# Kernel optimization log

Hardware: AMD Instinct MI355X
Metric: run time of the kernel (lower is better)

## Reference

```python
import jax, jax.numpy as jnp
import numpy as np

INF = 1e10
D_KEY = 64

def setup_inputs() -> dict:
    key = jax.random.key(0)
    k1, k2, k3 = jax.random.split(key, 3)
    B, S, D = 4, 4096, D_KEY
    return {
        "query": jax.random.normal(k1, (B, S, D), dtype=jnp.float32),
        "key": jax.random.normal(k2, (B, S, D), dtype=jnp.float32),
        "value": jax.random.normal(k3, (B, S, D), dtype=jnp.float32),
        "mask": jnp.ones((B, S), dtype=jnp.float32),
    }

def reference(query, key, value, mask):
    # dot_products: [B, Sq, Sk]
    dot = jnp.einsum('bqd,bkd->bqk', query, key)
    S = key.shape[1]
    # causal: subtract INF on strict upper triangle (triu(1))
    tri = jnp.triu(jnp.ones((S, S), dtype=dot.dtype), 1) * INF
    dot = dot - tri[None, :, :]
    # additive padding mask: subtract (1-mask)*INF broadcast over query dim
    dot = dot - (1.0 - mask)[:, None, :] * INF
    scale = jnp.sqrt(jnp.float32(D_KEY))
    probs = jax.nn.softmax(dot / scale, axis=-1)  # [B, Sq, Sk]
    # dropout ratio = 0.0 -> identity
    return jnp.einsum('bqk,bkd->bqd', probs, value)
```

## Files before the change

### kernel.cpp

```cpp
#include <hip/hip_runtime.h>
#include <hip/hip_bf16.h>


#define S_LEN  4096
#define N_B    4
#define NT64   64
#define BIGF   1.803368e9f
#define QSCALE (0.125f * 1.44269504089f)
#define FIXMAX 11.0f
#define BIGNEG 1.25e9f
#define MADD_PAD 4224

typedef __attribute__((ext_vector_type(8))) short short8;
typedef __attribute__((ext_vector_type(4))) float f32x4;
typedef __attribute__((ext_vector_type(2))) unsigned int uint2v;
typedef unsigned short ushort_t;

#define KT2_OFF   0
#define KT2_BYTES (N_B * NT64 * 4096 * 2)
#define VT2_OFF   (KT2_OFF + KT2_BYTES)
#define VT2_BYTES (N_B * NT64 * 4096 * 2)
#define NSLOT     (N_B * 368 * 4)
#define OP_OFF    (VT2_OFF + VT2_BYTES)
#define OP_BYTES  (NSLOT * 512 * 4)
#define PLS_OFF   (OP_OFF + OP_BYTES)
#define PLS_BYTES (NSLOT * 16 * 4)
#define MADD_OFF  (PLS_OFF + PLS_BYTES)
#define MADD_BYTES (N_B * MADD_PAD * 4)
#define FLAG_OFF  (MADD_OFF + MADD_BYTES)
#define WS5_NEEDED (FLAG_OFF + 64)

__device__ __forceinline__ unsigned short f2bf(float f) {
    union { float f; unsigned u; } v; v.f = f;
    unsigned r = v.u + 0x7FFF + ((v.u >> 16) & 1);
    return (unsigned short)(r >> 16);
}
__device__ __forceinline__ float bflo(unsigned u) {
    union { unsigned u; float f; } v; v.u = u << 16; return v.f;
}
__device__ __forceinline__ float bfhi(unsigned u) {
    union { unsigned u; float f; } v; v.u = u & 0xffff0000u; return v.f;
}
__device__ __forceinline__ void ld_lds16(const void* g, void* l) {
    __builtin_amdgcn_global_load_lds((const __attribute__((address_space(1))) void*)g,
                                     (__attribute__((address_space(3))) void*)l, 16, 0, 0);
}


__global__ __launch_bounds__(256)
void prep5(const float* __restrict__ K, const float* __restrict__ V,
           const float* __restrict__ M,
           ushort_t* __restrict__ Kt, ushort_t* __restrict__ Vt,
           float* __restrict__ Madd, unsigned* __restrict__ Flag)
{
    const int t = blockIdx.x, b = blockIdx.y, tid = threadIdx.x;
    ushort_t* ko = Kt + ((size_t)(b * NT64 + t)) * 4096;
    ushort_t* vo = Vt + ((size_t)(b * NT64 + t)) * 4096;
    #pragma unroll
    for (int i = 0; i < 2; ++i) {
        const int idx = tid + 256 * i;
        const int row = idx >> 3, cc = idx & 7;
        const float* src = K + ((size_t)(b * S_LEN + t * 64 + row)) * 64 + cc * 8;
        const f32x4 a = *(const f32x4*)src;
        const f32x4 d4 = *(const f32x4*)(src + 4);
        short8 w;
        w[0]=(short)f2bf(a[0]); w[1]=(short)f2bf(a[1]); w[2]=(short)f2bf(a[2]); w[3]=(short)f2bf(a[3]);
        w[4]=(short)f2bf(d4[0]); w[5]=(short)f2bf(d4[1]); w[6]=(short)f2bf(d4[2]); w[7]=(short)f2bf(d4[3]);
        *(short8*)(ko + row * 64 + ((cc ^ (row & 7)) << 3)) = w;
    }
    #pragma unroll
    for (int i = 0; i < 2; ++i) {
        const int idx = tid + 256 * i;
        const int cc = idx >> 6, d = idx & 63;
        short8 w;
        #pragma unroll
        for (int j = 0; j < 8; ++j)
            w[j] = (short)f2bf(V[((size_t)(b * S_LEN + t * 64 + cc * 8 + j)) * 64 + d]);
        *(short8*)(vo + d * 64 + ((cc ^ (d & 7)) << 3)) = w;
    }
    if (tid < 64) {
        const int k = t * 64 + tid;
        const float mv = M[b * S_LEN + k];
        Madd[b * MADD_PAD + k] = (1.0f - mv) * BIGF;
        const unsigned long long nz = __ballot(mv != 1.0f);
        if (tid == 0 && nz) atomicOr(Flag, 1u);
    }
}

#define PTRANS(PA, PB, PF) do {                                                     \
    unsigned c00_, c01_, c10_, c11_;                                                \
    __asm__("v_cvt_pk_bf16_f32 %0, %1, %2" : "=v"(c00_) : "v"(PA[0]), "v"(PA[1])); \
    __asm__("v_cvt_pk_bf16_f32 %0, %1, %2" : "=v"(c01_) : "v"(PA[2]), "v"(PA[3])); \
    __asm__("v_cvt_pk_bf16_f32 %0, %1, %2" : "=v"(c10_) : "v"(PB[0]), "v"(PB[1])); \
    __asm__("v_cvt_pk_bf16_f32 %0, %1, %2" : "=v"(c11_) : "v"(PB[2]), "v"(PB[3])); \
    uint2v s0_ = __builtin_amdgcn_permlane32_swap(c00_, c10_, false, false);        \
    uint2v s1_ = __builtin_amdgcn_permlane32_swap(c01_, c11_, false, false);        \
    const unsigned T0_ = (unsigned)__builtin_amdgcn_ds_swizzle((int)s0_.x, 0x401F); \
    const unsigned T1_ = (unsigned)__builtin_amdgcn_ds_swizzle((int)s1_.x, 0x401F); \
    const unsigned U0_ = (unsigned)__builtin_amdgcn_ds_swizzle((int)s0_.y, 0x401F); \
    const unsigned U1_ = (unsigned)__builtin_amdgcn_ds_swizzle((int)s1_.y, 0x401F); \
    union { unsigned u[4]; short8 s; } pw_;                                         \
    pw_.u[0] = evn ? s0_.x : U0_;                                                   \
    pw_.u[1] = evn ? s1_.x : U1_;                                                   \
    pw_.u[2] = evn ? T0_ : s0_.y;                                                   \
    pw_.u[3] = evn ? T1_ : s1_.y;                                                   \
    PF = pw_.s;                                                                     \
} while (0)

__global__ __launch_bounds__(256)
void attn_fa8(const float* __restrict__ Q, const ushort_t* __restrict__ Kt,
              const ushort_t* __restrict__ Vt, const float* __restrict__ Madd,
              const unsigned* __restrict__ Flag,
              unsigned* __restrict__ Opu, float* __restrict__ Pll,
              float* __restrict__ O)
{
    const int x = 373 - blockIdx.x;
    const int b = blockIdx.y;
    int v = 1;
    #pragma unroll
    for (int vv = 2; vv <= 11; ++vv) v += (x >= 3 * vv * (vv - 1)) ? 1 : 0;
    const int y  = x - 3 * v * (v - 1);
    const int T  = 6 * (v - 1) + y / v;
    const int c  = y - (y / v) * v;
    const int t0 = 6 * c;
    const int tmax = T + 1;
    const int t1 = (t0 + 6 < tmax) ? t0 + 6 : tmax;

    const unsigned anymask = *Flag;

    const int wid  = threadIdx.x >> 6;
    const int lane = threadIdx.x & 63, l15 = lane & 15, g = lane >> 4;
    const bool evn = ((lane & 16) == 0);
    const int qbase = T * 64 + wid * 16;

    __shared__ __attribute__((aligned(16))) ushort_t Kb[2][4096];
    __shared__ __attribute__((aligned(16))) ushort_t Vb[2][4096];

    const float* Qrow = Q + ((size_t)(b * S_LEN + qbase + l15)) * 64 + g * 8;
    const f32x4 qa = *(const f32x4*)(Qrow);
    const f32x4 qb_ = *(const f32x4*)(Qrow + 4);
    const f32x4 qc = *(const f32x4*)(Qrow + 32);
    const f32x4 qd = *(const f32x4*)(Qrow + 36);
    short8 qf0, qf1;
    #pragma unroll
    for (int j = 0; j < 4; ++j) {
        qf0[j]     = (short)f2bf(qa[j]  * QSCALE);
        qf0[4 + j] = (short)f2bf(qb_[j] * QSCALE);
        qf1[j]     = (short)f2bf(qc[j]  * QSCALE);
        qf1[4 + j] = (short)f2bf(qd[j]  * QSCALE);
    }
    short8 ones8;
    #pragma unroll
    for (int j = 0; j < 8; ++j) ones8[j] = (short)0x3F80;

    const char*  KtB = (const char*)Kt + (size_t)b * (NT64 * 8192);
    const char*  VtB = (const char*)Vt + (size_t)b * (NT64 * 8192);
    const float* MaB = Madd + (size_t)b * MADD_PAD + 4 * g;

    f32x4 acc[5];
    #pragma unroll
    for (int dt = 0; dt < 5; ++dt) acc[dt] = (f32x4){0.f, 0.f, 0.f, 0.f};

    auto stage = [&](int bf, int t_) {
        const char* kg = KtB + (size_t)t_ * 8192 + wid * 2048 + lane * 16;
        char* kl = (char*)&Kb[bf][0] + wid * 2048;
        ld_lds16(kg,        kl);
        ld_lds16(kg + 1024, kl + 1024);
        const char* vg = VtB + (size_t)t_ * 8192 + wid * 2048 + lane * 16;
        char* vl = (char*)&Vb[bf][0] + wid * 2048;
        ld_lds16(vg,        vl);
        ld_lds16(vg + 1024, vl + 1024);
    };

    stage(0, t0);
    int buf = 0;
    const int ch0 = ((g ^ (l15 & 7)) << 3);
    const int ch1 = (((4 | g) ^ (l15 & 7)) << 3);

    for (int t = t0; t < t1; ++t) {
        f32x4 mm0, mm1, mm2, mm3;
        if (anymask) {
            const float* mp = MaB + t * 64;
            mm0 = *(const f32x4*)(mp);
            mm1 = *(const f32x4*)(mp + 16);
            mm2 = *(const f32x4*)(mp + 32);
            mm3 = *(const f32x4*)(mp + 48);
        }
        if (t + 1 < t1) {
            stage(buf ^ 1, t + 1);
            __asm__ volatile("s_waitcnt vmcnt(4)" ::: "memory");
        } else {
            __asm__ volatile("s_waitcnt vmcnt(0)" ::: "memory");
        }
        __builtin_amdgcn_s_barrier();
        __builtin_amdgcn_sched_barrier(0);

        const ushort_t* kb = &Kb[buf][0];
        const f32x4 z_ = (f32x4){0.f, 0.f, 0.f, 0.f};
        short8 k00 = *(const short8*)(kb + ((0  + l15) << 6) + ch0);
        short8 k01 = *(const short8*)(kb + ((0  + l15) << 6) + ch1);
        short8 k10 = *(const short8*)(kb + ((16 + l15) << 6) + ch0);
        short8 k11 = *(const short8*)(kb + ((16 + l15) << 6) + ch1);
        short8 k20 = *(const short8*)(kb + ((32 + l15) << 6) + ch0);
        short8 k21 = *(const short8*)(kb + ((32 + l15) << 6) + ch1);
        short8 k30 = *(const short8*)(kb + ((48 + l15) << 6) + ch0);
        short8 k31 = *(const short8*)(kb + ((48 + l15) << 6) + ch1);
        f32x4 st0 = __builtin_amdgcn_mfma_f32_16x16x32_bf16(k00, qf0, z_, 0, 0, 0);
        f32x4 st1 = __builtin_amdgcn_mfma_f32_16x16x32_bf16(k10, qf0, z_, 0, 0, 0);
        f32x4 st2 = __builtin_amdgcn_mfma_f32_16x16x32_bf16(k20, qf0, z_, 0, 0, 0);
        f32x4 st3 = __builtin_amdgcn_mfma_f32_16x16x32_bf16(k30, qf0, z_, 0, 0, 0);
        st0 = __builtin_amdgcn_mfma_f32_16x16x32_bf16(k01, qf1, st0, 0, 0, 0);
        st1 = __builtin_amdgcn_mfma_f32_16x16x32_bf16(k11, qf1, st1, 0, 0, 0);
        st2 = __builtin_amdgcn_mfma_f32_16x16x32_bf16(k21, qf1, st2, 0, 0, 0);
        st3 = __builtin_amdgcn_mfma_f32_16x16x32_bf16(k31, qf1, st3, 0, 0, 0);

        if (anymask) {
            st0 -= mm0; st1 -= mm1; st2 -= mm2; st3 -= mm3;
        }
        if (t == T) {
            const int qg = 16 * wid + l15 - 4 * g;
            #pragma unroll
            for (int r = 0; r < 4; ++r) {
                if (r > qg)      st0[r] -= BIGF;
                if (16 + r > qg) st1[r] -= BIGF;
                if (32 + r > qg) st2[r] -= BIGF;
                if (48 + r > qg) st3[r] -= BIGF;
            }
        }

        float p0[4], p1[4], p2[4], p3[4];
        #pragma unroll
        for (int r = 0; r < 4; ++r) {
            p0[r] = exp2f(st0[r] - FIXMAX);
            p1[r] = exp2f(st1[r] - FIXMAX);
            p2[r] = exp2f(st2[r] - FIXMAX);
            p3[r] = exp2f(st3[r] - FIXMAX);
        }

        short8 pfA, pfB;
        PTRANS(p0, p1, pfA);
        PTRANS(p2, p3, pfB);

        const ushort_t* vb = &Vb[buf][0];
        short8 vA0 = *(const short8*)(vb + ((0  + l15) << 6) + ch0);
        short8 vB0 = *(const short8*)(vb + ((0  + l15) << 6) + ch1);
        short8 vA1 = *(const short8*)(vb + ((16 + l15) << 6) + ch0);
        short8 vB1 = *(const short8*)(vb + ((16 + l15) << 6) + ch1);
        short8 vA2 = *(const short8*)(vb + ((32 + l15) << 6) + ch0);
        short8 vB2 = *(const short8*)(vb + ((32 + l15) << 6) + ch1);
        short8 vA3 = *(const short8*)(vb + ((48 + l15) << 6) + ch0);
        short8 vB3 = *(const short8*)(vb + ((48 + l15) << 6) + ch1);
        __builtin_amdgcn_s_setprio(1);
        acc[0] = __builtin_amdgcn_mfma_f32_16x16x32_bf16(pfA, vA0, acc[0], 0, 0, 0);
        acc[1] = __builtin_amdgcn_mfma_f32_16x16x32_bf16(pfA, vA1, acc[1], 0, 0, 0);
        acc[2] = __builtin_amdgcn_mfma_f32_16x16x32_bf16(pfA, vA2, acc[2], 0, 0, 0);
        acc[3] = __builtin_amdgcn_mfma_f32_16x16x32_bf16(pfA, vA3, acc[3], 0, 0, 0);
        acc[4] = __builtin_amdgcn_mfma_f32_16x16x32_bf16(pfA, ones8, acc[4], 0, 0, 0);
        acc[0] = __builtin_amdgcn_mfma_f32_16x16x32_bf16(pfB, vB0, acc[0], 0, 0, 0);
        acc[1] = __builtin_amdgcn_mfma_f32_16x16x32_bf16(pfB, vB1, acc[1], 0, 0, 0);
        acc[2] = __builtin_amdgcn_mfma_f32_16x16x32_bf16(pfB, vB2, acc[2], 0, 0, 0);
        acc[3] = __builtin_amdgcn_mfma_f32_16x16x32_bf16(pfB, vB3, acc[3], 0, 0, 0);
        acc[4] = __builtin_amdgcn_mfma_f32_16x16x32_bf16(pfB, ones8, acc[4], 0, 0, 0);
        __builtin_amdgcn_s_setprio(0);

        __builtin_amdgcn_sched_barrier(0);
        __builtin_amdgcn_s_barrier();
        buf ^= 1;
    }

    if (v == 1) {
        float* Ob = O + ((size_t)(b * S_LEN + qbase)) * 64;
        #pragma unroll
        for (int r = 0; r < 4; ++r) {
            const float il = 1.0f / acc[4][r];
            #pragma unroll
            for (int dt = 0; dt < 4; ++dt)
                Ob[(4 * g + r) * 64 + 16 * dt + l15] = acc[dt][r] * il;
        }
    } else {
        const int slot = (b * 368 + (x - 6)) * 4 + wid;
        unsigned* Os = Opu + (size_t)slot * 512;
        #pragma unroll
        for (int dt = 0; dt < 4; ++dt) {
            unsigned plo, phi;
            __asm__("v_cvt_pk_bf16_f32 %0, %1, %2" : "=v"(plo) : "v"(acc[dt][0]), "v"(acc[dt][1]));
            __asm__("v_cvt_pk_bf16_f32 %0, %1, %2" : "=v"(phi) : "v"(acc[dt][2]), "v"(acc[dt][3]));
            *(uint2v*)&Os[(16 * dt + l15) * 8 + g * 2] = (uint2v){plo, phi};
        }
        if (l15 == 0) {
            #pragma unroll
            for (int r = 0; r < 4; ++r)
                Pll[slot * 16 + 4 * g + r] = acc[4][r];
        }
    }
}

__global__ __launch_bounds__(256)
void combine5(const unsigned* __restrict__ Opu, const float* __restrict__ Pll,
              float* __restrict__ O)
{
    const int bx = blockIdx.x, b = blockIdx.y;
    const int T = 6 + (bx >> 2), w = bx & 3;
    const int v = (T + 6) / 6;
    const int x0 = 3 * v * (v - 1) + (T - 6 * (v - 1)) * v;
    const int sb = (b * 368 + (x0 - 6)) * 4 + w;
    const int tid = threadIdx.x, rg = tid >> 6, d = tid & 63;

    float l[4] = {0.f, 0.f, 0.f, 0.f};
    float a[4] = {0.f, 0.f, 0.f, 0.f};
    for (int cc = 0; cc < v; ++cc) {
        const int sl = sb + 4 * cc;
        #pragma unroll
        for (int j = 0; j < 4; ++j)
            l[j] += Pll[sl * 16 + 4 * rg + j];
        const uint2v pu = *(const uint2v*)&Opu[(size_t)sl * 512 + d * 8 + rg * 2];
        a[0] += bflo(pu[0]);
        a[1] += bfhi(pu[0]);
        a[2] += bflo(pu[1]);
        a[3] += bfhi(pu[1]);
    }
    float* Ob = O + ((size_t)(b * S_LEN + T * 64 + w * 16 + 4 * rg)) * 64 + d;
    #pragma unroll
    for (int j = 0; j < 4; ++j)
        Ob[(size_t)j * 64] = a[j] / l[j];
}


__global__ __launch_bounds__(256)
void attn_fwd_fb(const float* __restrict__ Q, const float* __restrict__ K,
                 const float* __restrict__ V, const float* __restrict__ M,
                 float* __restrict__ O)
{
    const int tile  = blockIdx.x;
    const int b     = blockIdx.y;
    const int qbase = tile * 64;
    const int tid   = threadIdx.x;
    const int wave  = tid >> 6;
    const int lane  = tid & 63;
    const int l15   = lane & 15;
    const int g     = lane >> 4;

    __shared__ __attribute__((aligned(16))) unsigned short Klds[32 * 64];
    __shared__ __attribute__((aligned(16))) unsigned short Vtlds[64 * 40];
    __shared__ __attribute__((aligned(16))) unsigned short Plds[4][16 * 40];

    const float* Qb = Q + ((size_t)b * S_LEN + qbase) * 64;
    const float* Kb = K + (size_t)b * S_LEN * 64;
    const float* Vb = V + (size_t)b * S_LEN * 64;
    const float* Mb = M + (size_t)b * S_LEN;

    const int qrow = 16 * wave + l15;
    short8 qf[2];
    #pragma unroll
    for (int dc = 0; dc < 2; ++dc) {
        const float* src = Qb + (size_t)qrow * 64 + dc * 32 + g * 8;
        #pragma unroll
        for (int j = 0; j < 8; ++j) qf[dc][j] = (short)f2bf(src[j] * 0.125f);
    }

    f32x4 acc[4];
    #pragma unroll
    for (int dt = 0; dt < 4; ++dt) acc[dt] = (f32x4){0.f, 0.f, 0.f, 0.f};
    float mrow[4], lrow[4];
    #pragma unroll
    for (int r = 0; r < 4; ++r) { mrow[r] = -1e30f; lrow[r] = 0.f; }

    const int q_max_wave = qbase + 16 * wave + 15;
    const int nkv = (qbase + 64) / 32;

    for (int it = 0; it < nkv; ++it) {
        const int kv = it * 32;
        __syncthreads();
        {
            const int k = tid >> 3, c = tid & 7;
            const float* src = Kb + (size_t)(kv + k) * 64 + c * 8;
            short8 t8;
            #pragma unroll
            for (int j = 0; j < 8; ++j) t8[j] = (short)f2bf(src[j]);
            const int byte = k * 128 + ((c * 16) ^ ((k & 7) << 4));
            *(short8*)((char*)Klds + byte) = t8;
        }
        {
            const int k = tid & 31, dch = tid >> 5;
            const float* src = Vb + (size_t)(kv + k) * 64 + dch * 8;
            #pragma unroll
            for (int j = 0; j < 8; ++j)
                Vtlds[(dch * 8 + j) * 40 + k] = f2bf(src[j]);
        }
        __syncthreads();

        if (kv > q_max_wave) continue;

        f32x4 s[2];
        s[0] = (f32x4){0.f,0.f,0.f,0.f};
        s[1] = (f32x4){0.f,0.f,0.f,0.f};
        #pragma unroll
        for (int kt = 0; kt < 2; ++kt) {
            const int krow = 16 * kt + l15;
            #pragma unroll
            for (int dc = 0; dc < 2; ++dc) {
                const int byte = krow * 128 + ((dc * 64 + g * 16) ^ ((krow & 7) << 4));
                short8 kf = *(const short8*)((const char*)Klds + byte);
                s[kt] = __builtin_amdgcn_mfma_f32_16x16x32_bf16(qf[dc], kf, s[kt], 0, 0, 0);
            }
        }

        float mk0 = Mb[kv + l15];
        float mk1 = Mb[kv + 16 + l15];
        #pragma unroll
        for (int kt = 0; kt < 2; ++kt) {
            const int gk = kv + 16 * kt + l15;
            const float madd = (1.0f - (kt ? mk1 : mk0)) * BIGNEG;
            #pragma unroll
            for (int r = 0; r < 4; ++r) {
                const int gq = qbase + 16 * wave + 4 * g + r;
                float vv = s[kt][r] - madd;
                if (gk > gq) vv -= BIGNEG;
                s[kt][r] = vv;
            }
        }

        float pexp[2][4], alpha[4];
        #pragma unroll
        for (int r = 0; r < 4; ++r) {
            float tm = fmaxf(s[0][r], s[1][r]);
            #pragma unroll
            for (int off = 8; off >= 1; off >>= 1)
                tm = fmaxf(tm, __shfl_xor(tm, off, 64));
            const float mnew = fmaxf(mrow[r], tm);
            const float a  = __expf(mrow[r] - mnew);
            const float p0 = __expf(s[0][r] - mnew);
            const float p1 = __expf(s[1][r] - mnew);
            float rs = p0 + p1;
            #pragma unroll
            for (int off = 8; off >= 1; off >>= 1)
                rs += __shfl_xor(rs, off, 64);
            lrow[r] = lrow[r] * a + rs;
            mrow[r] = mnew;
            alpha[r] = a;
            pexp[0][r] = p0; pexp[1][r] = p1;
        }

        #pragma unroll
        for (int dt = 0; dt < 4; ++dt)
            #pragma unroll
            for (int r = 0; r < 4; ++r)
                acc[dt][r] *= alpha[r];

        unsigned short* P = Plds[wave];
        #pragma unroll
        for (int kt = 0; kt < 2; ++kt)
            #pragma unroll
            for (int r = 0; r < 4; ++r)
                P[(4 * g + r) * 40 + 16 * kt + l15] = f2bf(pexp[kt][r]);

        __asm__ volatile("s_waitcnt lgkmcnt(0)" ::: "memory");

        short8 pf = *(const short8*)((const char*)P + (l15 * 40 + g * 8) * 2);
        #pragma unroll
        for (int dt = 0; dt < 4; ++dt) {
            short8 vf = *(const short8*)((const char*)Vtlds + ((dt * 16 + l15) * 40 + g * 8) * 2);
            acc[dt] = __builtin_amdgcn_mfma_f32_16x16x32_bf16(pf, vf, acc[dt], 0, 0, 0);
        }
    }

    float* Ob = O + ((size_t)b * S_LEN + qbase) * 64;
    #pragma unroll
    for (int r = 0; r < 4; ++r) {
        const float inv = 1.0f / lrow[r];
        const int row = 16 * wave + 4 * g + r;
        #pragma unroll
        for (int dt = 0; dt < 4; ++dt)
            Ob[(size_t)row * 64 + dt * 16 + l15] = acc[dt][r] * inv;
    }
}

extern "C" void kernel_launch(void* const* d_in, const int* in_sizes, int n_in,
                              void* d_out, int out_size, void* d_ws, size_t ws_size,
                              hipStream_t stream) {
    const float* Q = (const float*)d_in[0];
    const float* K = (const float*)d_in[1];
    const float* V = (const float*)d_in[2];
    const float* M = (const float*)d_in[3];
    float* O = (float*)d_out;

    if (ws_size >= (size_t)WS5_NEEDED) {
        ushort_t* Kt = (ushort_t*)((char*)d_ws + KT2_OFF);
        ushort_t* Vt = (ushort_t*)((char*)d_ws + VT2_OFF);
        unsigned* Op = (unsigned*)((char*)d_ws + OP_OFF);
        float*    Pll= (float*)((char*)d_ws + PLS_OFF);
        float*    Ma = (float*)((char*)d_ws + MADD_OFF);
        unsigned* Fl = (unsigned*)((char*)d_ws + FLAG_OFF);
        hipMemsetAsync(Fl, 0, 4, stream);
        prep5<<<dim3(NT64, N_B), 256, 0, stream>>>(K, V, M, Kt, Vt, Ma, Fl);
        attn_fa8<<<dim3(374, N_B), 256, 0, stream>>>(Q, Kt, Vt, Ma, Fl, Op, Pll, O);
        combine5<<<dim3(232, N_B), 256, 0, stream>>>(Op, Pll, O);
    } else {
        dim3 grid(S_LEN / 64, N_B);
        attn_fwd_fb<<<grid, 256, 0, stream>>>(Q, K, V, M, O);
    }
}
```

Baseline: 45.59 us.

## Double query tile per block to 128 rows, halving grid and split slots

Each block now covers 128 query rows, with each wave holding two 16-row query fragments, so every K/V tile loaded into LDS serves twice as many queries. The grid and split-K schedule are rebuilt for 128-row tiles (187 blocks per batch, 184 partial slots). Waves whose diagonal tile has already been passed skip their compute through a liveness flag. The combine kernel is rewritten for the new partial layout. Register pressure rises with twice the accumulators, launch bounds now ask for 3 blocks per unit, and the grid has fewer blocks to spread across CUs.

```diff
diff --git a/kernel.cpp b/kernel.cpp
--- a/kernel.cpp
+++ b/kernel.cpp
@@ -14,21 +14,22 @@
 typedef __attribute__((ext_vector_type(8))) short short8;
 typedef __attribute__((ext_vector_type(4))) float f32x4;
 typedef __attribute__((ext_vector_type(2))) unsigned int uint2v;
+typedef __attribute__((ext_vector_type(4))) unsigned int uint4v;
 typedef unsigned short ushort_t;
 
 #define KT2_OFF   0
 #define KT2_BYTES (N_B * NT64 * 4096 * 2)
 #define VT2_OFF   (KT2_OFF + KT2_BYTES)
 #define VT2_BYTES (N_B * NT64 * 4096 * 2)
-#define NSLOT     (N_B * 368 * 4)
+#define NSLOT     (N_B * 184 * 4)
 #define OP_OFF    (VT2_OFF + VT2_BYTES)
-#define OP_BYTES  (NSLOT * 512 * 4)
+#define OP_BYTES  (NSLOT * 1024 * 4)
 #define PLS_OFF   (OP_OFF + OP_BYTES)
-#define PLS_BYTES (NSLOT * 16 * 4)
+#define PLS_BYTES (NSLOT * 32 * 4)
 #define MADD_OFF  (PLS_OFF + PLS_BYTES)
 #define MADD_BYTES (N_B * MADD_PAD * 4)
 #define FLAG_OFF  (MADD_OFF + MADD_BYTES)
-#define WS5_NEEDED (FLAG_OFF + 64)
+#define WS6_NEEDED (FLAG_OFF + 64)
 
 __device__ __forceinline__ unsigned short f2bf(float f) {
     union { float f; unsigned u; } v; v.f = f;
@@ -107,47 +108,67 @@
     PF = pw_.s;                                                                     \
 } while (0)
 
-__global__ __launch_bounds__(256)
-void attn_fa8(const float* __restrict__ Q, const ushort_t* __restrict__ Kt,
+#define CMASK(SV, BB, QG) do {                     \
+    _Pragma("unroll")                              \
+    for (int r_ = 0; r_ < 4; ++r_)                 \
+        if ((BB) + r_ > (QG)) SV[r_] -= BIGF;      \
+} while (0)
+
+__global__ __launch_bounds__(256, 3)
+void attn_fa9(const float* __restrict__ Q, const ushort_t* __restrict__ Kt,
               const ushort_t* __restrict__ Vt, const float* __restrict__ Madd,
               const unsigned* __restrict__ Flag,
               unsigned* __restrict__ Opu, float* __restrict__ Pll,
               float* __restrict__ O)
 {
-    const int x = 373 - blockIdx.x;
+    const int x = 186 - blockIdx.x;
     const int b = blockIdx.y;
     int v = 1;
     #pragma unroll
-    for (int vv = 2; vv <= 11; ++vv) v += (x >= 3 * vv * (vv - 1)) ? 1 : 0;
-    const int y  = x - 3 * v * (v - 1);
-    const int T  = 6 * (v - 1) + y / v;
+    for (int vv = 2; vv <= 11; ++vv) v += (x >= (3 * vv * (vv - 1)) / 2) ? 1 : 0;
+    const int y  = x - (3 * v * (v - 1)) / 2;
+    const int T  = 3 * (v - 1) + y / v;
     const int c  = y - (y / v) * v;
+    const int nt = 2 * T + 2;
     const int t0 = 6 * c;
-    const int tmax = T + 1;
-    const int t1 = (t0 + 6 < tmax) ? t0 + 6 : tmax;
+    const int t1 = (t0 + 6 < nt) ? t0 + 6 : nt;
 
     const unsigned anymask = *Flag;
 
     const int wid  = threadIdx.x >> 6;
     const int lane = threadIdx.x & 63, l15 = lane & 15, g = lane >> 4;
     const bool evn = ((lane & 16) == 0);
-    const int qbase = T * 64 + wid * 16;
+    const int qbase = T * 128 + wid * 32;
+    const int dtile = 2 * T + (wid >> 1);
+    const int qg0 = 32 * (wid & 1) + l15 - 4 * g;
+    const int qg1 = qg0 + 16;
 
     __shared__ __attribute__((aligned(16))) ushort_t Kb[2][4096];
     __shared__ __attribute__((aligned(16))) ushort_t Vb[2][4096];
 
-    const float* Qrow = Q + ((size_t)(b * S_LEN + qbase + l15)) * 64 + g * 8;
-    const f32x4 qa = *(const f32x4*)(Qrow);
-    const f32x4 qb_ = *(const f32x4*)(Qrow + 4);
-    const f32x4 qc = *(const f32x4*)(Qrow + 32);
-    const f32x4 qd = *(const f32x4*)(Qrow + 36);
-    short8 qf0, qf1;
-    #pragma unroll
-    for (int j = 0; j < 4; ++j) {
-        qf0[j]     = (short)f2bf(qa[j]  * QSCALE);
-        qf0[4 + j] = (short)f2bf(qb_[j] * QSCALE);
-        qf1[j]     = (short)f2bf(qc[j]  * QSCALE);
-        qf1[4 + j] = (short)f2bf(qd[j]  * QSCALE);
+    const float* Q0 = Q + ((size_t)(b * S_LEN + qbase + l15)) * 64 + g * 8;
+    short8 qA0, qA1, qB0, qB1;
+    {
+        const f32x4 a0 = *(const f32x4*)(Q0);
+        const f32x4 a1 = *(const f32x4*)(Q0 + 4);
+        const f32x4 a2 = *(const f32x4*)(Q0 + 32);
+        const f32x4 a3 = *(const f32x4*)(Q0 + 36);
+        const float* Q1 = Q0 + 16 * 64;
+        const f32x4 b0 = *(const f32x4*)(Q1);
+        const f32x4 b1 = *(const f32x4*)(Q1 + 4);
+        const f32x4 b2 = *(const f32x4*)(Q1 + 32);
+        const f32x4 b3 = *(const f32x4*)(Q1 + 36);
+        #pragma unroll
+        for (int j = 0; j < 4; ++j) {
+            qA0[j]     = (short)f2bf(a0[j] * QSCALE);
+            qA0[4 + j] = (short)f2bf(a1[j] * QSCALE);
+            qA1[j]     = (short)f2bf(a2[j] * QSCALE);
+            qA1[4 + j] = (short)f2bf(a3[j] * QSCALE);
+            qB0[j]     = (short)f2bf(b0[j] * QSCALE);
+            qB0[4 + j] = (short)f2bf(b1[j] * QSCALE);
+            qB1[j]     = (short)f2bf(b2[j] * QSCALE);
+            qB1[4 + j] = (short)f2bf(b3[j] * QSCALE);
+        }
     }
     short8 ones8;
     #pragma unroll
@@ -157,9 +178,12 @@
     const char*  VtB = (const char*)Vt + (size_t)b * (NT64 * 8192);
     const float* MaB = Madd + (size_t)b * MADD_PAD + 4 * g;
 
-    f32x4 acc[5];
-    #pragma unroll
-    for (int dt = 0; dt < 5; ++dt) acc[dt] = (f32x4){0.f, 0.f, 0.f, 0.f};
+    f32x4 accA[5], accB[5];
+    #pragma unroll
+    for (int dt = 0; dt < 5; ++dt) {
+        accA[dt] = (f32x4){0.f, 0.f, 0.f, 0.f};
+        accB[dt] = (f32x4){0.f, 0.f, 0.f, 0.f};
+    }
 
     auto stage = [&](int bf, int t_) {
         const char* kg = KtB + (size_t)t_ * 8192 + wid * 2048 + lane * 16;
@@ -178,8 +202,9 @@
     const int ch1 = (((4 | g) ^ (l15 & 7)) << 3);
 
     for (int t = t0; t < t1; ++t) {
+        const bool live = (t <= dtile);
         f32x4 mm0, mm1, mm2, mm3;
-        if (anymask) {
+        if (anymask && live) {
             const float* mp = MaB + t * 64;
             mm0 = *(const f32x4*)(mp);
             mm1 = *(const f32x4*)(mp + 16);
@@ -195,73 +220,98 @@
         __builtin_amdgcn_s_barrier();
         __builtin_amdgcn_sched_barrier(0);
 
-        const ushort_t* kb = &Kb[buf][0];
-        const f32x4 z_ = (f32x4){0.f, 0.f, 0.f, 0.f};
-        short8 k00 = *(const short8*)(kb + ((0  + l15) << 6) + ch0);
-        short8 k01 = *(const short8*)(kb + ((0  + l15) << 6) + ch1);
-        short8 k10 = *(const short8*)(kb + ((16 + l15) << 6) + ch0);
-        short8 k11 = *(const short8*)(kb + ((16 + l15) << 6) + ch1);
-        short8 k20 = *(const short8*)(kb + ((32 + l15) << 6) + ch0);
-        short8 k21 = *(const short8*)(kb + ((32 + l15) << 6) + ch1);
-        short8 k30 = *(const short8*)(kb + ((48 + l15) << 6) + ch0);
-        short8 k31 = *(const short8*)(kb + ((48 + l15) << 6) + ch1);
-        f32x4 st0 = __builtin_amdgcn_mfma_f32_16x16x32_bf16(k00, qf0, z_, 0, 0, 0);
-        f32x4 st1 = __builtin_amdgcn_mfma_f32_16x16x32_bf16(k10, qf0, z_, 0, 0, 0);
-        f32x4 st2 = __builtin_amdgcn_mfma_f32_16x16x32_bf16(k20, qf0, z_, 0, 0, 0);
-        f32x4 st3 = __builtin_amdgcn_mfma_f32_16x16x32_bf16(k30, qf0, z_, 0, 0, 0);
-        st0 = __builtin_amdgcn_mfma_f32_16x16x32_bf16(k01, qf1, st0, 0, 0, 0);
-        st1 = __builtin_amdgcn_mfma_f32_16x16x32_bf16(k11, qf1, st1, 0, 0, 0);
-        st2 = __builtin_amdgcn_mfma_f32_16x16x32_bf16(k21, qf1, st2, 0, 0, 0);
-        st3 = __builtin_amdgcn_mfma_f32_16x16x32_bf16(k31, qf1, st3, 0, 0, 0);
-
-        if (anymask) {
-            st0 -= mm0; st1 -= mm1; st2 -= mm2; st3 -= mm3;
-        }
-        if (t == T) {
-            const int qg = 16 * wid + l15 - 4 * g;
+        if (live) {
+            const ushort_t* kb = &Kb[buf][0];
+            const f32x4 z_ = (f32x4){0.f, 0.f, 0.f, 0.f};
+            short8 k00 = *(const short8*)(kb + ((0  + l15) << 6) + ch0);
+            short8 k01 = *(const short8*)(kb + ((0  + l15) << 6) + ch1);
+            short8 k10 = *(const short8*)(kb + ((16 + l15) << 6) + ch0);
+            short8 k11 = *(const short8*)(kb + ((16 + l15) << 6) + ch1);
+            short8 k20 = *(const short8*)(kb + ((32 + l15) << 6) + ch0);
+            short8 k21 = *(const short8*)(kb + ((32 + l15) << 6) + ch1);
+            short8 k30 = *(const short8*)(kb + ((48 + l15) << 6) + ch0);
+            short8 k31 = *(const short8*)(kb + ((48 + l15) << 6) + ch1);
+
+            f32x4 sA0 = __builtin_amdgcn_mfma_f32_16x16x32_bf16(k00, qA0, z_, 0, 0, 0);
+            f32x4 sA1 = __builtin_amdgcn_mfma_f32_16x16x32_bf16(k10, qA0, z_, 0, 0, 0);
+            f32x4 sA2 = __builtin_amdgcn_mfma_f32_16x16x32_bf16(k20, qA0, z_, 0, 0, 0);
+            f32x4 sA3 = __builtin_amdgcn_mfma_f32_16x16x32_bf16(k30, qA0, z_, 0, 0, 0);
+            f32x4 sB0 = __builtin_amdgcn_mfma_f32_16x16x32_bf16(k00, qB0, z_, 0, 0, 0);
+            f32x4 sB1 = __builtin_amdgcn_mfma_f32_16x16x32_bf16(k10, qB0, z_, 0, 0, 0);
+            f32x4 sB2 = __builtin_amdgcn_mfma_f32_16x16x32_bf16(k20, qB0, z_, 0, 0, 0);
+            f32x4 sB3 = __builtin_amdgcn_mfma_f32_16x16x32_bf16(k30, qB0, z_, 0, 0, 0);
+            sA0 = __builtin_amdgcn_mfma_f32_16x16x32_bf16(k01, qA1, sA0, 0, 0, 0);
+            sA1 = __builtin_amdgcn_mfma_f32_16x16x32_bf16(k11, qA1, sA1, 0, 0, 0);
+            sA2 = __builtin_amdgcn_mfma_f32_16x16x32_bf16(k21, qA1, sA2, 0, 0, 0);
+            sA3 = __builtin_amdgcn_mfma_f32_16x16x32_bf16(k31, qA1, sA3, 0, 0, 0);
+            sB0 = __builtin_amdgcn_mfma_f32_16x16x32_bf16(k01, qB1, sB0, 0, 0, 0);
+            sB1 = __builtin_amdgcn_mfma_f32_16x16x32_bf16(k11, qB1, sB1, 0, 0, 0);
+            sB2 = __builtin_amdgcn_mfma_f32_16x16x32_bf16(k21, qB1, sB2, 0, 0, 0);
+            sB3 = __builtin_amdgcn_mfma_f32_16x16x32_bf16(k31, qB1, sB3, 0, 0, 0);
+
+            if (anymask) {
+                sA0 -= mm0; sA1 -= mm1; sA2 -= mm2; sA3 -= mm3;
+                sB0 -= mm0; sB1 -= mm1; sB2 -= mm2; sB3 -= mm3;
+            }
+            if (t == dtile) {
+                CMASK(sA0, 0, qg0); CMASK(sA1, 16, qg0);
+                CMASK(sA2, 32, qg0); CMASK(sA3, 48, qg0);
+                CMASK(sB0, 0, qg1); CMASK(sB1, 16, qg1);
+                CMASK(sB2, 32, qg1); CMASK(sB3, 48, qg1);
+            }
+
+            float pa0[4], pa1[4], pa2[4], pa3[4];
+            float pb0[4], pb1[4], pb2[4], pb3[4];
             #pragma unroll
             for (int r = 0; r < 4; ++r) {
-                if (r > qg)      st0[r] -= BIGF;
-                if (16 + r > qg) st1[r] -= BIGF;
-                if (32 + r > qg) st2[r] -= BIGF;
-                if (48 + r > qg) st3[r] -= BIGF;
-            }
-        }
-
-        float p0[4], p1[4], p2[4], p3[4];
-        #pragma unroll
-        for (int r = 0; r < 4; ++r) {
-            p0[r] = exp2f(st0[r] - FIXMAX);
-            p1[r] = exp2f(st1[r] - FIXMAX);
-            p2[r] = exp2f(st2[r] - FIXMAX);
-            p3[r] = exp2f(st3[r] - FIXMAX);
-        }
-
-        short8 pfA, pfB;
-        PTRANS(p0, p1, pfA);
-        PTRANS(p2, p3, pfB);
-
-        const ushort_t* vb = &Vb[buf][0];
-        short8 vA0 = *(const short8*)(vb + ((0  + l15) << 6) + ch0);
-        short8 vB0 = *(const short8*)(vb + ((0  + l15) << 6) + ch1);
-        short8 vA1 = *(const short8*)(vb + ((16 + l15) << 6) + ch0);
-        short8 vB1 = *(const short8*)(vb + ((16 + l15) << 6) + ch1);
-        short8 vA2 = *(const short8*)(vb + ((32 + l15) << 6) + ch0);
-        short8 vB2 = *(const short8*)(vb + ((32 + l15) << 6) + ch1);
-        short8 vA3 = *(const short8*)(vb + ((48 + l15) << 6) + ch0);
-        short8 vB3 = *(const short8*)(vb + ((48 + l15) << 6) + ch1);
-        __builtin_amdgcn_s_setprio(1);
-        acc[0] = __builtin_amdgcn_mfma_f32_16x16x32_bf16(pfA, vA0, acc[0], 0, 0, 0);
-        acc[1] = __builtin_amdgcn_mfma_f32_16x16x32_bf16(pfA, vA1, acc[1], 0, 0, 0);
-        acc[2] = __builtin_amdgcn_mfma_f32_16x16x32_bf16(pfA, vA2, acc[2], 0, 0, 0);
-        acc[3] = __builtin_amdgcn_mfma_f32_16x16x32_bf16(pfA, vA3, acc[3], 0, 0, 0);
-        acc[4] = __builtin_amdgcn_mfma_f32_16x16x32_bf16(pfA, ones8, acc[4], 0, 0, 0);
-        acc[0] = __builtin_amdgcn_mfma_f32_16x16x32_bf16(pfB, vB0, acc[0], 0, 0, 0);
-        acc[1] = __builtin_amdgcn_mfma_f32_16x16x32_bf16(pfB, vB1, acc[1], 0, 0, 0);
-        acc[2] = __builtin_amdgcn_mfma_f32_16x16x32_bf16(pfB, vB2, acc[2], 0, 0, 0);
-        acc[3] = __builtin_amdgcn_mfma_f32_16x16x32_bf16(pfB, vB3, acc[3], 0, 0, 0);
-        acc[4] = __builtin_amdgcn_mfma_f32_16x16x32_bf16(pfB, ones8, acc[4], 0, 0, 0);
-        __builtin_amdgcn_s_setprio(0);
+                pa0[r] = exp2f(sA0[r] - FIXMAX);
+                pa1[r] = exp2f(sA1[r] - FIXMAX);
+                pa2[r] = exp2f(sA2[r] - FIXMAX);
+                pa3[r] = exp2f(sA3[r] - FIXMAX);
+                pb0[r] = exp2f(sB0[r] - FIXMAX);
+                pb1[r] = exp2f(sB1[r] - FIXMAX);
+                pb2[r] = exp2f(sB2[r] - FIXMAX);
+                pb3[r] = exp2f(sB3[r] - FIXMAX);
+            }
+
+            short8 pAlo, pAhi, pBlo, pBhi;
+            PTRANS(pa0, pa1, pAlo);
+            PTRANS(pa2, pa3, pAhi);
+            PTRANS(pb0, pb1, pBlo);
+            PTRANS(pb2, pb3, pBhi);
+
+            const ushort_t* vb = &Vb[buf][0];
+            short8 vL0 = *(const short8*)(vb + ((0  + l15) << 6) + ch0);
+            short8 vH0 = *(const short8*)(vb + ((0  + l15) << 6) + ch1);
+            short8 vL1 = *(const short8*)(vb + ((16 + l15) << 6) + ch0);
+            short8 vH1 = *(const short8*)(vb + ((16 + l15) << 6) + ch1);
+            short8 vL2 = *(const short8*)(vb + ((32 + l15) << 6) + ch0);
+            short8 vH2 = *(const short8*)(vb + ((32 + l15) << 6) + ch1);
+            short8 vL3 = *(const short8*)(vb + ((48 + l15) << 6) + ch0);
+            short8 vH3 = *(const short8*)(vb + ((48 + l15) << 6) + ch1);
+            __builtin_amdgcn_s_setprio(1);
+            accA[0] = __builtin_amdgcn_mfma_f32_16x16x32_bf16(pAlo, vL0, accA[0], 0, 0, 0);
+            accA[1] = __builtin_amdgcn_mfma_f32_16x16x32_bf16(pAlo, vL1, accA[1], 0, 0, 0);
+            accA[2] = __builtin_amdgcn_mfma_f32_16x16x32_bf16(pAlo, vL2, accA[2], 0, 0, 0);
+            accA[3] = __builtin_amdgcn_mfma_f32_16x16x32_bf16(pAlo, vL3, accA[3], 0, 0, 0);
+            accA[4] = __builtin_amdgcn_mfma_f32_16x16x32_bf16(pAlo, ones8, accA[4], 0, 0, 0);
+            accB[0] = __builtin_amdgcn_mfma_f32_16x16x32_bf16(pBlo, vL0, accB[0], 0, 0, 0);
+            accB[1] = __builtin_amdgcn_mfma_f32_16x16x32_bf16(pBlo, vL1, accB[1], 0, 0, 0);
+            accB[2] = __builtin_amdgcn_mfma_f32_16x16x32_bf16(pBlo, vL2, accB[2], 0, 0, 0);
+            accB[3] = __builtin_amdgcn_mfma_f32_16x16x32_bf16(pBlo, vL3, accB[3], 0, 0, 0);
+            accB[4] = __builtin_amdgcn_mfma_f32_16x16x32_bf16(pBlo, ones8, accB[4], 0, 0, 0);
+            accA[0] = __builtin_amdgcn_mfma_f32_16x16x32_bf16(pAhi, vH0, accA[0], 0, 0, 0);
+            accA[1] = __builtin_amdgcn_mfma_f32_16x16x32_bf16(pAhi, vH1, accA[1], 0, 0, 0);
+            accA[2] = __builtin_amdgcn_mfma_f32_16x16x32_bf16(pAhi, vH2, accA[2], 0, 0, 0);
+            accA[3] = __builtin_amdgcn_mfma_f32_16x16x32_bf16(pAhi, vH3, accA[3], 0, 0, 0);
+            accA[4] = __builtin_amdgcn_mfma_f32_16x16x32_bf16(pAhi, ones8, accA[4], 0, 0, 0);
+            accB[0] = __builtin_amdgcn_mfma_f32_16x16x32_bf16(pBhi, vH0, accB[0], 0, 0, 0);
+            accB[1] = __builtin_amdgcn_mfma_f32_16x16x32_bf16(pBhi, vH1, accB[1], 0, 0, 0);
+            accB[2] = __builtin_amdgcn_mfma_f32_16x16x32_bf16(pBhi, vH2, accB[2], 0, 0, 0);
+            accB[3] = __builtin_amdgcn_mfma_f32_16x16x32_bf16(pBhi, vH3, accB[3], 0, 0, 0);
+            accB[4] = __builtin_amdgcn_mfma_f32_16x16x32_bf16(pBhi, ones8, accB[4], 0, 0, 0);
+            __builtin_amdgcn_s_setprio(0);
+        }
 
         __builtin_amdgcn_sched_barrier(0);
         __builtin_amdgcn_s_barrier();
@@ -272,56 +322,73 @@
         float* Ob = O + ((size_t)(b * S_LEN + qbase)) * 64;
         #pragma unroll
         for (int r = 0; r < 4; ++r) {
-            const float il = 1.0f / acc[4][r];
-            #pragma unroll
-            for (int dt = 0; dt < 4; ++dt)
-                Ob[(4 * g + r) * 64 + 16 * dt + l15] = acc[dt][r] * il;
+            const float ila = 1.0f / accA[4][r];
+            const float ilb = 1.0f / accB[4][r];
+            #pragma unroll
+            for (int dt = 0; dt < 4; ++dt) {
+                Ob[(4 * g + r) * 64 + 16 * dt + l15]        = accA[dt][r] * ila;
+                Ob[(16 + 4 * g + r) * 64 + 16 * dt + l15]   = accB[dt][r] * ilb;
+            }
         }
     } else {
-        const int slot = (b * 368 + (x - 6)) * 4 + wid;
-        unsigned* Os = Opu + (size_t)slot * 512;
+        const int slot = (b * 184 + (x - 3)) * 4 + wid;
+        unsigned* Os = Opu + (size_t)slot * 1024;
         #pragma unroll
         for (int dt = 0; dt < 4; ++dt) {
-            unsigned plo, phi;
-            __asm__("v_cvt_pk_bf16_f32 %0, %1, %2" : "=v"(plo) : "v"(acc[dt][0]), "v"(acc[dt][1]));
-            __asm__("v_cvt_pk_bf16_f32 %0, %1, %2" : "=v"(phi) : "v"(acc[dt][2]), "v"(acc[dt][3]));
-            *(uint2v*)&Os[(16 * dt + l15) * 8 + g * 2] = (uint2v){plo, phi};
+            unsigned u0, u1, u2, u3;
+            __asm__("v_cvt_pk_bf16_f32 %0, %1, %2" : "=v"(u0) : "v"(accA[dt][0]), "v"(accA[dt][1]));
+            __asm__("v_cvt_pk_bf16_f32 %0, %1, %2" : "=v"(u1) : "v"(accA[dt][2]), "v"(accA[dt][3]));
+            __asm__("v_cvt_pk_bf16_f32 %0, %1, %2" : "=v"(u2) : "v"(accB[dt][0]), "v"(accB[dt][1]));
+            __asm__("v_cvt_pk_bf16_f32 %0, %1, %2" : "=v"(u3) : "v"(accB[dt][2]), "v"(accB[dt][3]));
+            const int d = 16 * dt + l15;
+            Os[(2 * g + 0) * 64 + d] = u0;
+            Os[(2 * g + 1) * 64 + d] = u1;
+            Os[(8 + 2 * g + 0) * 64 + d] = u2;
+            Os[(8 + 2 * g + 1) * 64 + d] = u3;
         }
         if (l15 == 0) {
             #pragma unroll
-            for (int r = 0; r < 4; ++r)
-                Pll[slot * 16 + 4 * g + r] = acc[4][r];
+            for (int r = 0; r < 4; ++r) {
+                Pll[slot * 32 + 4 * g + r]      = accA[4][r];
+                Pll[slot * 32 + 16 + 4 * g + r] = accB[4][r];
+            }
         }
     }
 }
 
 __global__ __launch_bounds__(256)
-void combine5(const unsigned* __restrict__ Opu, const float* __restrict__ Pll,
+void combine6(const unsigned* __restrict__ Opu, const float* __restrict__ Pll,
               float* __restrict__ O)
 {
     const int bx = blockIdx.x, b = blockIdx.y;
-    const int T = 6 + (bx >> 2), w = bx & 3;
-    const int v = (T + 6) / 6;
-    const int x0 = 3 * v * (v - 1) + (T - 6 * (v - 1)) * v;
-    const int sb = (b * 368 + (x0 - 6)) * 4 + w;
+    const int T = 3 + (bx >> 2), wv = bx & 3;
+    const int v = (T + 3) / 3;
+    const int x0 = (3 * v * (v - 1)) / 2 + (T - 3 * (v - 1)) * v;
+    const int sb = (b * 184 + (x0 - 3)) * 4 + wv;
     const int tid = threadIdx.x, rg = tid >> 6, d = tid & 63;
 
-    float l[4] = {0.f, 0.f, 0.f, 0.f};
-    float a[4] = {0.f, 0.f, 0.f, 0.f};
+    float a[8] = {0.f,0.f,0.f,0.f,0.f,0.f,0.f,0.f};
+    float l[8] = {0.f,0.f,0.f,0.f,0.f,0.f,0.f,0.f};
     for (int cc = 0; cc < v; ++cc) {
         const int sl = sb + 4 * cc;
-        #pragma unroll
-        for (int j = 0; j < 4; ++j)
-            l[j] += Pll[sl * 16 + 4 * rg + j];
-        const uint2v pu = *(const uint2v*)&Opu[(size_t)sl * 512 + d * 8 + rg * 2];
-        a[0] += bflo(pu[0]);
-        a[1] += bfhi(pu[0]);
-        a[2] += bflo(pu[1]);
-        a[3] += bfhi(pu[1]);
-    }
-    float* Ob = O + ((size_t)(b * S_LEN + T * 64 + w * 16 + 4 * rg)) * 64 + d;
-    #pragma unroll
-    for (int j = 0; j < 4; ++j)
+        const uint4v pu = *(const uint4v*)&Opu[(size_t)sl * 1024 + (4 * rg) * 64 + d];
+        const unsigned* base = &Opu[(size_t)sl * 1024 + d];
+        const unsigned w0 = base[(4 * rg + 0) * 64];
+        const unsigned w1 = base[(4 * rg + 1) * 64];
+        const unsigned w2 = base[(4 * rg + 2) * 64];
+        const unsigned w3 = base[(4 * rg + 3) * 64];
+        (void)pu;
+        a[0] += bflo(w0); a[1] += bfhi(w0);
+        a[2] += bflo(w1); a[3] += bfhi(w1);
+        a[4] += bflo(w2); a[5] += bfhi(w2);
+        a[6] += bflo(w3); a[7] += bfhi(w3);
+        #pragma unroll
+        for (int j = 0; j < 8; ++j)
+            l[j] += Pll[sl * 32 + 8 * rg + j];
+    }
+    float* Ob = O + ((size_t)(b * S_LEN + T * 128 + wv * 32 + 8 * rg)) * 64 + d;
+    #pragma unroll
+    for (int j = 0; j < 8; ++j)
         Ob[(size_t)j * 64] = a[j] / l[j];
 }
 
@@ -484,7 +551,7 @@
     const float* M = (const float*)d_in[3];
     float* O = (float*)d_out;
 
-    if (ws_size >= (size_t)WS5_NEEDED) {
+    if (ws_size >= (size_t)WS6_NEEDED) {
         ushort_t* Kt = (ushort_t*)((char*)d_ws + KT2_OFF);
         ushort_t* Vt = (ushort_t*)((char*)d_ws + VT2_OFF);
         unsigned* Op = (unsigned*)((char*)d_ws + OP_OFF);
@@ -493,8 +560,8 @@
         unsigned* Fl = (unsigned*)((char*)d_ws + FLAG_OFF);
         hipMemsetAsync(Fl, 0, 4, stream);
         prep5<<<dim3(NT64, N_B), 256, 0, stream>>>(K, V, M, Kt, Vt, Ma, Fl);
-        attn_fa8<<<dim3(374, N_B), 256, 0, stream>>>(Q, Kt, Vt, Ma, Fl, Op, Pll, O);
-        combine5<<<dim3(232, N_B), 256, 0, stream>>>(Op, Pll, O);
+        attn_fa9<<<dim3(187, N_B), 256, 0, stream>>>(Q, Kt, Vt, Ma, Fl, Op, Pll, O);
+        combine6<<<dim3(116, N_B), 256, 0, stream>>>(Op, Pll, O);
     } else {
         dim3 grid(S_LEN / 64, N_B);
         attn_fwd_fb<<<grid, 256, 0, stream>>>(Q, K, V, M, O);
```

Result: faster. 44.39 us (-2.6%).
